# Optimization experiments

Measured on AMD Instinct MI355X. Metric: run time of the kernel, lower is better.

The kernel has to match this reference:

```python
import jax, jax.numpy as jnp
import numpy as np
import math

GAIN = 6.0
FREQ = 1000.0
Q = 0.707
SAMPLE_RATE = 44100


def _peaking_coeffs():
    # torchaudio.functional.equalizer_biquad coefficients (peaking EQ)
    w0 = 2.0 * math.pi * FREQ / SAMPLE_RATE
    A = math.exp(GAIN / 40.0 * math.log(10.0))
    alpha = math.sin(w0) / (2.0 * Q)
    b0 = 1.0 + alpha * A
    b1 = -2.0 * math.cos(w0)
    b2 = 1.0 - alpha * A
    a0 = 1.0 + alpha / A
    a1 = -2.0 * math.cos(w0)
    a2 = 1.0 - alpha / A
    # normalize by a0 (lfilter semantics)
    return (np.float32(b0 / a0), np.float32(b1 / a0), np.float32(b2 / a0),
            np.float32(a1 / a0), np.float32(a2 / a0))


def setup_inputs() -> dict:
    key = jax.random.key(0)
    x = jax.random.normal(key, (8, 2, 1200000), dtype=jnp.float32)
    return {"x": x}


def _biquad(x):
    # x: [B, C, T]; direct-form-I biquad with zero initial conditions
    b0, b1, b2, a1, a2 = _peaking_coeffs()
    # FIR part, fully vectorized: f[n] = b0*x[n] + b1*x[n-1] + b2*x[n-2]
    xp = jnp.pad(x, ((0, 0), (0, 0), (2, 0)))
    f = b0 * xp[..., 2:] + b1 * xp[..., 1:-1] + b2 * xp[..., :-2]
    # IIR part via scan over time: y[n] = f[n] - a1*y[n-1] - a2*y[n-2]
    f_t = jnp.moveaxis(f, -1, 0)  # [T, B, C]
    y0 = jnp.zeros(x.shape[:-1], dtype=x.dtype)

    def step(carry, ft):
        y1, y2 = carry
        y = ft - a1 * y1 - a2 * y2
        return (y, y1), y

    _, ys = jax.lax.scan(step, (y0, y0), f_t)
    return jnp.moveaxis(ys, 0, -1)  # [B, C, T]


def reference(x):
    return _biquad(x)
```

## Files before the change

kernel.cpp:

```cpp
#include <hip/hip_runtime.h>
#include <math.h>


#define T_LEN 1200000
#define NCH   16
#define L     32
#define NR    64
#define NWARM 4
#define OUT_ROWS (NR - NWARM)
#define OUT_PER_BLOCK (OUT_ROWS * L)
#define SEGS (T_LEN / OUT_PER_BLOCK)
#define STAGE_FLOATS (NR * L)

struct Params {
    float b0, b1, b2, a1, a2;
    float lnr, theta, inv_sinth;
    float C[6][4];
};

__global__ __launch_bounds__(64) void eq_kernel(const float* __restrict__ x,
                                                float* __restrict__ y, Params P)
{
    __shared__ __align__(16) float xs[STAGE_FLOATS];
    __shared__ float alpha[NR], beta[NR];
    __shared__ __align__(16) float c1t[L];
    __shared__ __align__(16) float c2t[L];

    const int lane = threadIdx.x;
    const int seg  = blockIdx.x;
    const int ch   = blockIdx.y;
    const float* __restrict__ xc = x + (size_t)ch * T_LEN;
    float*       __restrict__ yc = y + (size_t)ch * T_LEN;
    const int g0 = seg * OUT_PER_BLOCK - NWARM * L;

    if (lane < L) {
        int t = lane;
        float pht   = expf(t * P.lnr) * sinf((t + 1) * P.theta) * P.inv_sinth;
        float phtm1 = (t == 0) ? 0.f
                               : expf((t - 1) * P.lnr) * sinf(t * P.theta) * P.inv_sinth;
        c1t[t] = -P.a1 * pht - P.a2 * phtm1;
        c2t[t] = -P.a2 * pht;
    }

    #pragma unroll
    for (int it = 0; it < STAGE_FLOATS / 4 / 64; ++it) {
        int v = it * 64 + lane;
        int q = v << 2;
        int g = g0 + q;
        float4 val = make_float4(0.f, 0.f, 0.f, 0.f);
        if (g >= 0 && g < T_LEN) val = *(const float4*)(xc + g);
        int row = q >> 5, j = q & 31, m = row & 31, base = row << 5;
        xs[base + ((j + 0) ^ m)] = val.x;
        xs[base + ((j + 1) ^ m)] = val.y;
        xs[base + ((j + 2) ^ m)] = val.z;
        xs[base + ((j + 3) ^ m)] = val.w;
    }
    __syncthreads();

    float v1 = 0.f, v2 = 0.f;
    {
        const int row = lane, m = row & 31, base = row << 5;
        float x1, x2;
        if (row > 0) {
            int pb = (row - 1) << 5;
            int pm = (row - 1) & 31;
            x1 = xs[pb + (31 ^ pm)];
            x2 = xs[pb + (30 ^ pm)];
        } else { x1 = 0.f; x2 = 0.f; }
        #pragma unroll 8
        for (int j = 0; j < L; ++j) {
            int w = base + (j ^ m);
            float xv = xs[w];
            float f  = fmaf(P.b0, xv, fmaf(P.b1, x1, P.b2 * x2));
            float t2 = fmaf(-P.a2, v2, f);
            float yv = fmaf(-P.a1, v1, t2);
            v2 = v1; v1 = yv;
            x2 = x1; x1 = xv;
            xs[w] = yv;
        }
    }

    #pragma unroll
    for (int k = 0; k < 6; ++k) {
        int d = 1 << k;
        float p1 = __shfl_up(v1, d);
        float p2 = __shfl_up(v2, d);
        if (lane < d) { p1 = 0.f; p2 = 0.f; }
        float n1 = fmaf(P.C[k][0], p1, fmaf(P.C[k][1], p2, v1));
        float n2 = fmaf(P.C[k][2], p1, fmaf(P.C[k][3], p2, v2));
        v1 = n1; v2 = n2;
    }
    {
        float a_ = __shfl_up(v1, 1);
        float b_ = __shfl_up(v2, 1);
        if (lane == 0) { a_ = 0.f; b_ = 0.f; }
        alpha[lane] = a_; beta[lane] = b_;
    }
    __syncthreads();

    for (int vo = lane; vo < OUT_PER_BLOCK / 4; vo += 64) {
        int q = (vo << 2) + NWARM * L;
        int row = q >> 5, j = q & 31, m = row & 31, base = row << 5;
        float al = alpha[row], be = beta[row];
        float4 c1v = *(const float4*)&c1t[j];
        float4 c2v = *(const float4*)&c2t[j];
        float4 o4;
        o4.x = fmaf(al, c1v.x, fmaf(be, c2v.x, xs[base + ((j + 0) ^ m)]));
        o4.y = fmaf(al, c1v.y, fmaf(be, c2v.y, xs[base + ((j + 1) ^ m)]));
        o4.z = fmaf(al, c1v.z, fmaf(be, c2v.z, xs[base + ((j + 2) ^ m)]));
        o4.w = fmaf(al, c1v.w, fmaf(be, c2v.w, xs[base + ((j + 3) ^ m)]));
        *(float4*)(yc + g0 + q) = o4;
    }
}

extern "C" void kernel_launch(void* const* d_in, const int* in_sizes, int n_in,
                              void* d_out, int out_size, void* d_ws, size_t ws_size,
                              hipStream_t stream) {
    const float* x = (const float*)d_in[0];
    float* y = (float*)d_out;

    double w0    = 2.0 * M_PI * 1000.0 / 44100.0;
    double A     = exp(6.0 / 40.0 * log(10.0));
    double al    = sin(w0) / (2.0 * 0.707);
    double b0 = 1.0 + al * A;
    double b1 = -2.0 * cos(w0);
    double b2 = 1.0 - al * A;
    double a0 = 1.0 + al / A;
    double a1 = -2.0 * cos(w0);
    double a2 = 1.0 - al / A;
    b0 /= a0; b1 /= a0; b2 /= a0; a1 /= a0; a2 /= a0;

    Params P;
    P.b0 = (float)b0; P.b1 = (float)b1; P.b2 = (float)b2;
    P.a1 = (float)a1; P.a2 = (float)a2;

    double r     = sqrt(a2);
    double theta = acos(-a1 / (2.0 * r));
    P.lnr = (float)log(r);
    P.theta = (float)theta;
    P.inv_sinth = (float)(1.0 / sin(theta));

    double m00 = -a1, m01 = -a2, m10 = 1.0, m11 = 0.0;
    for (int s = 0; s < 5; ++s) {
        double t00 = m00 * m00 + m01 * m10;
        double t01 = m00 * m01 + m01 * m11;
        double t10 = m10 * m00 + m11 * m10;
        double t11 = m10 * m01 + m11 * m11;
        m00 = t00; m01 = t01; m10 = t10; m11 = t11;
    }
    for (int k = 0; k < 6; ++k) {
        P.C[k][0] = (float)m00; P.C[k][1] = (float)m01;
        P.C[k][2] = (float)m10; P.C[k][3] = (float)m11;
        double t00 = m00 * m00 + m01 * m10;
        double t01 = m00 * m01 + m01 * m11;
        double t10 = m10 * m00 + m11 * m10;
        double t11 = m10 * m01 + m11 * m11;
        m00 = t00; m01 = t01; m10 = t10; m11 = t11;
    }

    dim3 grid(SEGS, NCH);
    eq_kernel<<<grid, 64, 0, stream>>>(x, y, P);
}
```

Measured before the change: 35.32 us.

## Pack four independent wave segments per block and drop barriers via shuffles

Each 256-thread block now holds four independent 64-lane wavefronts, each handling its own segment in a private LDS slice. Block-wide __syncthreads barriers are replaced by compiler memory fences, which relies on each segment being handled by a single wavefront. The carry-in values alpha/beta are passed with __shfl instead of through shared memory, and each lane computes its own correction coefficients in registers instead of reading LDS tables. This removes barrier and LDS round-trip costs and raises per-CU occupancy, at the cost of redundant transcendental math per lane and a dependence on wavefront-64 execution without a real fence.

```diff
diff --git a/kernel.cpp b/kernel.cpp
--- a/kernel.cpp
+++ b/kernel.cpp
@@ -8,9 +8,11 @@
 #define NR    64
 #define NWARM 4
 #define OUT_ROWS (NR - NWARM)
-#define OUT_PER_BLOCK (OUT_ROWS * L)
-#define SEGS (T_LEN / OUT_PER_BLOCK)
-#define STAGE_FLOATS (NR * L)
+#define OUT_PER_SEG (OUT_ROWS * L)
+#define SEGS (T_LEN / OUT_PER_SEG)
+#define WAVE_FLOATS (NR * L)
+#define WPB   4
+#define NBLOCKS (SEGS * NCH / WPB)
 
 struct Params {
     float b0, b1, b2, a1, a2;
@@ -18,34 +20,42 @@
     float C[6][4];
 };
 
-__global__ __launch_bounds__(64) void eq_kernel(const float* __restrict__ x,
-                                                float* __restrict__ y, Params P)
+__global__ __launch_bounds__(256, 5) void eq_kernel(const float* __restrict__ x,
+                                                    float* __restrict__ y, Params P)
 {
-    __shared__ __align__(16) float xs[STAGE_FLOATS];
-    __shared__ float alpha[NR], beta[NR];
-    __shared__ __align__(16) float c1t[L];
-    __shared__ __align__(16) float c2t[L];
+    __shared__ __align__(16) float lds[WPB * WAVE_FLOATS];
 
-    const int lane = threadIdx.x;
-    const int seg  = blockIdx.x;
-    const int ch   = blockIdx.y;
+    const int lane = threadIdx.x & 63;
+    const int wid  = threadIdx.x >> 6;
+    float* __restrict__ xs = lds + (wid << 11);
+
+    const int wg  = blockIdx.x * WPB + wid;
+    const int ch  = wg / SEGS;
+    const int seg = wg - ch * SEGS;
     const float* __restrict__ xc = x + (size_t)ch * T_LEN;
     float*       __restrict__ yc = y + (size_t)ch * T_LEN;
-    const int g0 = seg * OUT_PER_BLOCK - NWARM * L;
+    const int g0 = seg * OUT_PER_SEG - NWARM * L;
 
-    if (lane < L) {
-        int t = lane;
-        float pht   = expf(t * P.lnr) * sinf((t + 1) * P.theta) * P.inv_sinth;
-        float phtm1 = (t == 0) ? 0.f
-                               : expf((t - 1) * P.lnr) * sinf(t * P.theta) * P.inv_sinth;
-        c1t[t] = -P.a1 * pht - P.a2 * phtm1;
-        c2t[t] = -P.a2 * pht;
+    float c1r[4], c2r[4];
+    {
+        const int t0 = (lane << 2) & 31;
+        float ph[5];
+        #pragma unroll
+        for (int k = 0; k < 5; ++k) {
+            int t = t0 - 1 + k;
+            ph[k] = (t < 0) ? 0.f
+                            : expf(t * P.lnr) * sinf((t + 1) * P.theta) * P.inv_sinth;
+        }
+        #pragma unroll
+        for (int k = 0; k < 4; ++k) {
+            c1r[k] = fmaf(-P.a1, ph[k + 1], -P.a2 * ph[k]);
+            c2r[k] = -P.a2 * ph[k + 1];
+        }
     }
 
     #pragma unroll
-    for (int it = 0; it < STAGE_FLOATS / 4 / 64; ++it) {
-        int v = it * 64 + lane;
-        int q = v << 2;
+    for (int it = 0; it < WAVE_FLOATS / 4 / 64; ++it) {
+        int q = ((it << 6) + lane) << 2;
         int g = g0 + q;
         float4 val = make_float4(0.f, 0.f, 0.f, 0.f);
         if (g >= 0 && g < T_LEN) val = *(const float4*)(xc + g);
@@ -55,18 +65,18 @@
         xs[base + ((j + 2) ^ m)] = val.z;
         xs[base + ((j + 3) ^ m)] = val.w;
     }
-    __syncthreads();
+    asm volatile("" ::: "memory");
 
     float v1 = 0.f, v2 = 0.f;
     {
-        const int row = lane, m = row & 31, base = row << 5;
-        float x1, x2;
-        if (row > 0) {
-            int pb = (row - 1) << 5;
-            int pm = (row - 1) & 31;
+        const int m = lane & 31, base = lane << 5;
+        float x1 = 0.f, x2 = 0.f;
+        if (lane > 0) {
+            int pb = (lane - 1) << 5, pm = (lane - 1) & 31;
             x1 = xs[pb + (31 ^ pm)];
             x2 = xs[pb + (30 ^ pm)];
-        } else { x1 = 0.f; x2 = 0.f; }
+        }
+        asm volatile("" ::: "memory");
         #pragma unroll 8
         for (int j = 0; j < L; ++j) {
             int w = base + (j ^ m);
@@ -90,26 +100,29 @@
         float n2 = fmaf(P.C[k][2], p1, fmaf(P.C[k][3], p2, v2));
         v1 = n1; v2 = n2;
     }
-    {
-        float a_ = __shfl_up(v1, 1);
-        float b_ = __shfl_up(v2, 1);
-        if (lane == 0) { a_ = 0.f; b_ = 0.f; }
-        alpha[lane] = a_; beta[lane] = b_;
-    }
-    __syncthreads();
+    float e1 = __shfl_up(v1, 1);
+    float e2 = __shfl_up(v2, 1);
+    if (lane == 0) { e1 = 0.f; e2 = 0.f; }
+    asm volatile("" ::: "memory");
 
-    for (int vo = lane; vo < OUT_PER_BLOCK / 4; vo += 64) {
-        int q = (vo << 2) + NWARM * L;
-        int row = q >> 5, j = q & 31, m = row & 31, base = row << 5;
-        float al = alpha[row], be = beta[row];
-        float4 c1v = *(const float4*)&c1t[j];
-        float4 c2v = *(const float4*)&c2t[j];
-        float4 o4;
-        o4.x = fmaf(al, c1v.x, fmaf(be, c2v.x, xs[base + ((j + 0) ^ m)]));
-        o4.y = fmaf(al, c1v.y, fmaf(be, c2v.y, xs[base + ((j + 1) ^ m)]));
-        o4.z = fmaf(al, c1v.z, fmaf(be, c2v.z, xs[base + ((j + 2) ^ m)]));
-        o4.w = fmaf(al, c1v.w, fmaf(be, c2v.w, xs[base + ((j + 3) ^ m)]));
-        *(float4*)(yc + g0 + q) = o4;
+    const int j = (lane << 2) & 31;
+    #pragma unroll
+    for (int it = 0; it < 8; ++it) {
+        int vo = (it << 6) + lane;
+        int row = 4 + (it << 3) + (lane >> 3);
+        row = row > 63 ? 63 : row;
+        float al = __shfl(e1, row);
+        float be = __shfl(e2, row);
+        if (vo < OUT_PER_SEG / 4) {
+            int m = row & 31, base = row << 5;
+            float4 o;
+            o.x = fmaf(al, c1r[0], fmaf(be, c2r[0], xs[base + ((j + 0) ^ m)]));
+            o.y = fmaf(al, c1r[1], fmaf(be, c2r[1], xs[base + ((j + 1) ^ m)]));
+            o.z = fmaf(al, c1r[2], fmaf(be, c2r[2], xs[base + ((j + 2) ^ m)]));
+            o.w = fmaf(al, c1r[3], fmaf(be, c2r[3], xs[base + ((j + 3) ^ m)]));
+            int q = (vo << 2) + NWARM * L;
+            *(float4*)(yc + g0 + q) = o;
+        }
     }
 }
 
@@ -158,6 +171,5 @@
         m00 = t00; m01 = t01; m10 = t10; m11 = t11;
     }
 
-    dim3 grid(SEGS, NCH);
-    eq_kernel<<<grid, 64, 0, stream>>>(x, y, P);
+    eq_kernel<<<NBLOCKS, 256, 0, stream>>>(x, y, P);
 }
```

Result: no change. 35.36 us (+0.1%).
